# Optimization experiments

Hardware: AMD Instinct MI355X
Metric: run time of the kernel (lower is better)

Reference implementation:

```python
import jax, jax.numpy as jnp
import numpy as np

B, L, D = 2, 256, 256  # batch, length, raw feature dim (W dims are D+1)

def setup_inputs() -> dict:
    key = jax.random.key(0)
    k1, k2, k3, kw = jax.random.split(key, 4)
    layer1 = jax.random.normal(k1, (B, L, D), dtype=jnp.float32)
    layer2 = jax.random.normal(k2, (B, L, D), dtype=jnp.float32)
    layer3 = jax.random.normal(k3, (B, L, D), dtype=jnp.float32)
    # xavier_normal_ for a 3D tensor: fan_in = D+1 * (D+1) receptive? torch treats
    # dim0 as fan_out-ish; we just use a matched-scale gaussian (correctness of the
    # contraction math is what matters for the kernel baseline).
    std = float(np.sqrt(2.0 / ((D + 1) + (D + 1) * (D + 1))))
    W = jax.random.normal(kw, (D + 1, D + 1, D + 1), dtype=jnp.float32) * std
    return {"layer1": layer1, "layer2": layer2, "layer3": layer3, "W": W}

def _append_ones(x):
    ones = jnp.ones(x.shape[:2] + (1,), dtype=x.dtype)
    return jnp.concatenate([x, ones], axis=-1)

def reference(layer1, layer2, layer3, W):
    l1 = _append_ones(layer1)  # [n, L, a]
    l2 = _append_ones(layer2)  # [n, L, b]
    l3 = _append_ones(layer3)  # [n, L, c]
    # Chained contraction: nia,abc -> nibc ; nibc,njb -> nijc ; nijc,nkc -> nijk
    t = jnp.einsum('nia,abc->nibc', l1, W)
    t = jnp.einsum('nibc,njb->nijc', t, l2)
    out = jnp.einsum('nijc,nkc->nijk', t, l3)
    return out
```

## Files before the change

kernel.cpp:

```cpp
#include <hip/hip_runtime.h>

typedef unsigned short u16;
typedef __attribute__((ext_vector_type(8))) short bf16x8;
typedef __attribute__((ext_vector_type(4))) float f32x4;

#define GLOAD_LDS16(gsrc, ldst)                                               \
  __builtin_amdgcn_global_load_lds(                                           \
      (const __attribute__((address_space(1))) void*)(gsrc),                  \
      (__attribute__((address_space(3))) void*)(ldst), 16, 0, 0)

#define LDSOFF(p) \
  ((unsigned)(uintptr_t)(__attribute__((address_space(3))) const void*)(p))

#define SB0 __builtin_amdgcn_sched_barrier(0)

__device__ __forceinline__ u16 f2bf(float x) {
  unsigned u = __float_as_uint(x);
  u = (u + 0x7FFFu + ((u >> 16) & 1u)) >> 16;
  return (u16)u;
}

__global__ void prep_l_kernel(const float* __restrict__ l1,
                              const float* __restrict__ l2,
                              const float* __restrict__ l3,
                              u16* __restrict__ o1, u16* __restrict__ o2,
                              u16* __restrict__ o3) {
  int idx = blockIdx.x * 256 + threadIdx.x;
  const int NR = 512 * 288;
  if (idx >= 3 * NR) return;
  int which = idx / NR, rem = idx - which * NR;
  int r = rem / 288, p = rem - r * 288;
  const float* s = which == 0 ? l1 : which == 1 ? l2 : l3;
  u16* d = which == 0 ? o1 : which == 1 ? o2 : o3;
  float v = (p < 256) ? s[r * 256 + p] : (p == 256 ? 1.0f : 0.0f);
  d[rem] = f2bf(v);
}

__global__ void prep_w_kernel(const float* __restrict__ W, u16* __restrict__ W2) {
  __shared__ float tile[32][33];
  const int a0 = blockIdx.x * 32, c0 = blockIdx.y * 32, b = blockIdx.z;
  const int t = threadIdx.x;
#pragma unroll
  for (int p = 0; p < 4; ++p) {
    int idx = t + p * 256;
    int cl = idx & 31, r = idx >> 5;
    int a = a0 + r, c = c0 + cl;
    float v = 0.0f;
    if (a < 257 && b < 257 && c < 257) v = W[((long)a * 257 + b) * 257 + c];
    tile[r][cl] = v;
  }
  __syncthreads();
#pragma unroll
  for (int p = 0; p < 4; ++p) {
    int idx = t + p * 256;
    int al = idx & 31, ccl = idx >> 5;
    W2[((long)(c0 + ccl) * 288 + b) * 288 + (a0 + al)] = f2bf(tile[al][ccl]);
  }
}

__global__ __launch_bounds__(256, 4) void gemm_nt(
    const u16* __restrict__ A, const u16* __restrict__ B, u16* __restrict__ C,
    int K, int lda, int ldb, int ldc) {
  __shared__ u16 As[2][4096];
  __shared__ u16 Bs[2][4096];
  const int t = threadIdx.x;
  const int bid = blockIdx.x;
  const int xcd = bid & 7, sq = bid >> 3;
  const int nt = xcd * 81 + (sq >> 2);
  const int mt = sq & 3;
  const int m0 = mt * 128, n0 = nt * 128;
  const int lane = t & 63;
  const int w = t >> 6;
  const int wr = (w >> 1) * 64, wc = (w & 1) * 64;
  const int r16 = lane & 15;
  const int cgrp = lane >> 4;
  const int rr = cgrp * 4;
  const unsigned ABase = LDSOFF(&As[0][0]);
  const unsigned BBase = LDSOFF(&Bs[0][0]);
  (void)K;

  const u16* PA = A + (long)m0 * lda;
  const u16* PB = B + (long)n0 * ldb;

#define STG(buf, k0)                                                          \
  {                                                                           \
    _Pragma("unroll") for (int _p = 0; _p < 2; ++_p) {                        \
      int _q = t + _p * 256;                                                  \
      int _r = _q >> 2, _g = (_q & 3) ^ ((_r >> 1) & 3);                      \
      GLOAD_LDS16(PA + (long)_r * lda + (k0) + _g * 8, &As[buf][_q * 8]);     \
      GLOAD_LDS16(PB + (long)_r * ldb + (k0) + _g * 8, &Bs[buf][_q * 8]);     \
    }                                                                         \
  }

  f32x4 acc[4][4];
  const f32x4 zero = {0.f, 0.f, 0.f, 0.f};
#pragma unroll
  for (int i = 0; i < 4; ++i)
#pragma unroll
    for (int j = 0; j < 4; ++j) acc[i][j] = zero;

  STG(0, 0);

#define GCOL(NI)                                                              \
  __builtin_amdgcn_s_setprio(1);                                              \
  acc[0][NI] = __builtin_amdgcn_mfma_f32_16x16x32_bf16(af[0], bf[NI], acc[0][NI], 0, 0, 0); \
  acc[1][NI] = __builtin_amdgcn_mfma_f32_16x16x32_bf16(af[1], bf[NI], acc[1][NI], 0, 0, 0); \
  acc[2][NI] = __builtin_amdgcn_mfma_f32_16x16x32_bf16(af[2], bf[NI], acc[2][NI], 0, 0, 0); \
  acc[3][NI] = __builtin_amdgcn_mfma_f32_16x16x32_bf16(af[3], bf[NI], acc[3][NI], 0, 0, 0); \
  __builtin_amdgcn_s_setprio(0);                                              \
  SB0;

#define GSTEP(KS, NW)                                                         \
  {                                                                           \
    if ((KS) < 8) STG(((KS) + 1) & 1, ((KS) + 1) * 32);                       \
    asm volatile("s_waitcnt vmcnt(" #NW ")" ::: "memory");                    \
    SB0;                                                                      \
    __builtin_amdgcn_s_barrier();                                             \
    SB0;                                                                      \
    bf16x8 af[4], bf[4];                                                      \
    _Pragma("unroll") for (int mi = 0; mi < 4; ++mi) {                        \
      int R = wr + mi * 16 + r16;                                             \
      unsigned ao = ABase + (unsigned)(((((KS) & 1) * 4096) + R * 32 +        \
                                       ((cgrp ^ ((R >> 1) & 3)) * 8)) * 2);   \
      asm volatile("ds_read_b128 %0, %1" : "=v"(af[mi]) : "v"(ao));           \
    }                                                                         \
    _Pragma("unroll") for (int ni = 0; ni < 4; ++ni) {                        \
      int R = wc + ni * 16 + r16;                                             \
      unsigned ao = BBase + (unsigned)(((((KS) & 1) * 4096) + R * 32 +        \
                                       ((cgrp ^ ((R >> 1) & 3)) * 8)) * 2);   \
      asm volatile("ds_read_b128 %0, %1" : "=v"(bf[ni]) : "v"(ao));           \
    }                                                                         \
    SB0;                                                                      \
    asm volatile("s_waitcnt lgkmcnt(3)" ::: "memory"); SB0;                   \
    GCOL(0)                                                                   \
    asm volatile("s_waitcnt lgkmcnt(2)" ::: "memory"); SB0;                   \
    GCOL(1)                                                                   \
    asm volatile("s_waitcnt lgkmcnt(1)" ::: "memory"); SB0;                   \
    GCOL(2)                                                                   \
    asm volatile("s_waitcnt lgkmcnt(0)" ::: "memory"); SB0;                   \
    GCOL(3)                                                                   \
  }

  GSTEP(0, 4) GSTEP(1, 4) GSTEP(2, 4) GSTEP(3, 4) GSTEP(4, 4)
  GSTEP(5, 4) GSTEP(6, 4) GSTEP(7, 4) GSTEP(8, 0)
#undef GSTEP
#undef GCOL
#undef STG

#pragma unroll
  for (int mi = 0; mi < 4; ++mi) {
    int gm = m0 + wr + mi * 16 + rr;
#pragma unroll
    for (int ni = 0; ni < 4; ++ni) {
      int gc = n0 + wc + ni * 16 + r16;
#pragma unroll
      for (int r = 0; r < 4; ++r)
        C[(long)(gm + r) * ldc + gc] = f2bf(acc[mi][ni][r]);
    }
  }
}

__global__ __launch_bounds__(512, 2) void fused23(
    const u16* __restrict__ l2b, const u16* __restrict__ l3b,
    const u16* __restrict__ T1, float* __restrict__ out) {
  __shared__ u16 S[128 * 296];
  __shared__ u16 Bst[4][288 * 32];
  const int t = threadIdx.x;
  const int lane = t & 63;
  const int w = t >> 6;

  const int bid = blockIdx.x;
  const int xcd = bid & 7;
  const int seq = bid >> 3;
  const int ni = xcd * 64 + (seq >> 1);
  const int half = seq & 1;
  const int n = ni >> 8;

  const int r16 = lane & 15;
  const int cgrp = lane >> 4;
  const int kb = cgrp * 8;
  const int rr = cgrp * 4;
  const f32x4 zero = {0.f, 0.f, 0.f, 0.f};

  const u16* A2 = l2b + (long)n * 73728 + (long)(half * 128) * 288;
  const u16* BT = T1 + (long)ni * 82944;
  const u16* B3 = l3b + (long)n * 73728;
  const unsigned BOF = LDSOFF(&Bst[0][0]);
  const unsigned SOF = LDSOFF(&S[0]);

#define ISSUE_A(buf, kk)                                                      \
  {                                                                           \
    int q1 = w * 144 + lane;                                                  \
    int r1 = q1 >> 2, g1 = (q1 & 3) ^ ((r1 >> 1) & 3);                        \
    GLOAD_LDS16(BT + (long)r1 * 288 + (kk) * 32 + g1 * 8, &Bst[(buf)][q1 * 8]); \
    int q2 = q1 + 64;                                                         \
    int r2 = q2 >> 2, g2 = (q2 & 3) ^ ((r2 >> 1) & 3);                        \
    GLOAD_LDS16(BT + (long)r2 * 288 + (kk) * 32 + g2 * 8, &Bst[(buf)][q2 * 8]); \
    if (lane < 16) {                                                          \
      int q3 = w * 144 + 128 + lane;                                          \
      int r3 = q3 >> 2, g3 = (q3 & 3) ^ ((r3 >> 1) & 3);                      \
      GLOAD_LDS16(BT + (long)r3 * 288 + (kk) * 32 + g3 * 8, &Bst[(buf)][q3 * 8]); \
    }                                                                         \
  }
#define ISSUE_B(buf, kk)                                                      \
  {                                                                           \
    int q1 = w * 128 + lane;                                                  \
    int r1 = q1 >> 2, g1 = (q1 & 3) ^ ((r1 >> 1) & 3);                        \
    GLOAD_LDS16(B3 + (long)r1 * 288 + (kk) * 32 + g1 * 8, &Bst[(buf)][q1 * 8]); \
    int q2 = q1 + 64;                                                         \
    int r2 = q2 >> 2, g2 = (q2 & 3) ^ ((r2 >> 1) & 3);                        \
    GLOAD_LDS16(B3 + (long)r2 * 288 + (kk) * 32 + g2 * 8, &Bst[(buf)][q2 * 8]); \
  }

  {
    const int wm = w & 3, wn = w >> 2;
    f32x4 acc[2][9];
#pragma unroll
    for (int i = 0; i < 2; ++i)
#pragma unroll
      for (int j = 0; j < 9; ++j) acc[i][j] = zero;

    bf16x8 afr[18];
#pragma unroll
    for (int k = 0; k < 9; ++k)
#pragma unroll
      for (int mi = 0; mi < 2; ++mi)
        afr[k * 2 + mi] = *(const bf16x8*)(A2 +
            (long)(wm * 32 + mi * 16 + r16) * 288 + k * 32 + kb);
    SB0;

    ISSUE_A(0, 0);
    ISSUE_A(1, 1);

#define FA_MM(NJ)                                                             \
  __builtin_amdgcn_s_setprio(1);                                              \
  acc[0][NJ] = __builtin_amdgcn_mfma_f32_16x16x32_bf16(afc0, bf[NJ], acc[0][NJ], 0, 0, 0); \
  acc[1][NJ] = __builtin_amdgcn_mfma_f32_16x16x32_bf16(afc1, bf[NJ], acc[1][NJ], 0, 0, 0); \
  __builtin_amdgcn_s_setprio(0);

#define FA_STEP(K, NW)                                                        \
  {                                                                           \
    if ((K) + 2 <= 8) ISSUE_A(((K) + 2) & 3, (K) + 2);                        \
    asm volatile("s_waitcnt vmcnt(" #NW ")" ::: "memory");                    \
    SB0;                                                                      \
    __builtin_amdgcn_s_barrier();                                             \
    SB0;                                                                      \
    bf16x8 bf[9];                                                             \
    _Pragma("unroll") for (int nj = 0; nj < 9; ++nj) {                        \
      const int R = wn * 144 + nj * 16 + r16;                                 \
      unsigned ao = BOF + (unsigned)((((K) & 3) * 9216 + R * 32 +             \
                                      ((cgrp ^ ((R >> 1) & 3)) * 8)) * 2);    \
      asm volatile("ds_read_b128 %0, %1" : "=v"(bf[nj]) : "v"(ao));           \
    }                                                                         \
    SB0;                                                                      \
    const bf16x8 afc0 = afr[(K) * 2 + 0], afc1 = afr[(K) * 2 + 1];            \
    asm volatile("s_waitcnt lgkmcnt(6)" ::: "memory"); SB0;                   \
    FA_MM(0) FA_MM(1) FA_MM(2) SB0;                                           \
    asm volatile("s_waitcnt lgkmcnt(3)" ::: "memory"); SB0;                   \
    FA_MM(3) FA_MM(4) FA_MM(5) SB0;                                           \
    asm volatile("s_waitcnt lgkmcnt(0)" ::: "memory"); SB0;                   \
    FA_MM(6) FA_MM(7) FA_MM(8) SB0;                                           \
  }
    FA_STEP(0, 6) FA_STEP(1, 6) FA_STEP(2, 6) FA_STEP(3, 6) FA_STEP(4, 6)
    FA_STEP(5, 6) FA_STEP(6, 6) FA_STEP(7, 3) FA_STEP(8, 0)
#undef FA_STEP
#undef FA_MM

    __syncthreads();
    ISSUE_B(0, 0);
    ISSUE_B(1, 1);
#pragma unroll
    for (int mi = 0; mi < 2; ++mi)
#pragma unroll
      for (int nj = 0; nj < 9; ++nj)
#pragma unroll
        for (int q = 0; q < 4; ++q)
          S[(wm * 32 + mi * 16 + rr + q) * 296 + wn * 144 + nj * 16 + r16] =
              f2bf(acc[mi][nj][q]);
  }
  __syncthreads();

  {
    const int wm = w & 1, wn = w >> 1;
    f32x4 acc[4][4];
#pragma unroll
    for (int i = 0; i < 4; ++i)
#pragma unroll
      for (int j = 0; j < 4; ++j) acc[i][j] = zero;

#define FB_MM(NI)                                                             \
  __builtin_amdgcn_s_setprio(1);                                              \
  acc[0][NI] = __builtin_amdgcn_mfma_f32_16x16x32_bf16(af[0], bf[NI], acc[0][NI], 0, 0, 0); \
  acc[1][NI] = __builtin_amdgcn_mfma_f32_16x16x32_bf16(af[1], bf[NI], acc[1][NI], 0, 0, 0); \
  acc[2][NI] = __builtin_amdgcn_mfma_f32_16x16x32_bf16(af[2], bf[NI], acc[2][NI], 0, 0, 0); \
  acc[3][NI] = __builtin_amdgcn_mfma_f32_16x16x32_bf16(af[3], bf[NI], acc[3][NI], 0, 0, 0); \
  __builtin_amdgcn_s_setprio(0);                                              \
  SB0;

#define FB_STEP(K, NW)                                                        \
  {                                                                           \
    if ((K) + 2 <= 8) ISSUE_B(((K) + 2) & 3, (K) + 2);                        \
    asm volatile("s_waitcnt vmcnt(" #NW ")" ::: "memory");                    \
    SB0;                                                                      \
    __builtin_amdgcn_s_barrier();                                             \
    SB0;                                                                      \
    bf16x8 af[4], bf[4];                                                      \
    _Pragma("unroll") for (int mi = 0; mi < 4; ++mi) {                        \
      unsigned ao = SOF + (unsigned)(((wm * 64 + mi * 16 + r16) * 296 +       \
                                      (K) * 32 + kb) * 2);                    \
      asm volatile("ds_read_b128 %0, %1" : "=v"(af[mi]) : "v"(ao));           \
    }                                                                         \
    _Pragma("unroll") for (int nj = 0; nj < 4; ++nj) {                        \
      const int R = wn * 64 + nj * 16 + r16;                                  \
      unsigned ao = BOF + (unsigned)((((K) & 3) * 9216 + R * 32 +             \
                                      ((cgrp ^ ((R >> 1) & 3)) * 8)) * 2);    \
      asm volatile("ds_read_b128 %0, %1" : "=v"(bf[nj]) : "v"(ao));           \
    }                                                                         \
    SB0;                                                                      \
    asm volatile("s_waitcnt lgkmcnt(3)" ::: "memory"); SB0;                   \
    FB_MM(0)                                                                  \
    asm volatile("s_waitcnt lgkmcnt(2)" ::: "memory"); SB0;                   \
    FB_MM(1)                                                                  \
    asm volatile("s_waitcnt lgkmcnt(1)" ::: "memory"); SB0;                   \
    FB_MM(2)                                                                  \
    asm volatile("s_waitcnt lgkmcnt(0)" ::: "memory"); SB0;                   \
    FB_MM(3)                                                                  \
  }
    FB_STEP(0, 4) FB_STEP(1, 4) FB_STEP(2, 4) FB_STEP(3, 4) FB_STEP(4, 4)
    FB_STEP(5, 4) FB_STEP(6, 4) FB_STEP(7, 2) FB_STEP(8, 0)
#undef FB_STEP
#undef FB_MM

    float* O = out + (long)ni * 65536 + (long)(half * 128 + wm * 64) * 256 + wn * 64;
#pragma unroll
    for (int mi = 0; mi < 4; ++mi)
#pragma unroll
      for (int nj = 0; nj < 4; ++nj)
#pragma unroll
        for (int q = 0; q < 4; ++q)
          O[(long)(mi * 16 + rr + q) * 256 + nj * 16 + r16] = acc[mi][nj][q];
  }
#undef ISSUE_A
#undef ISSUE_B
}

extern "C" void kernel_launch(void* const* d_in, const int* in_sizes, int n_in,
                              void* d_out, int out_size, void* d_ws, size_t ws_size,
                              hipStream_t stream) {
  const float* l1 = (const float*)d_in[0];
  const float* l2 = (const float*)d_in[1];
  const float* l3 = (const float*)d_in[2];
  const float* W = (const float*)d_in[3];
  float* out = (float*)d_out;
  char* ws = (char*)d_ws;

  const long LB = 512L * 288 * 2;
  u16* l1b = (u16*)ws;
  u16* l2b = (u16*)(ws + LB);
  u16* l3b = (u16*)(ws + 2 * LB);
  u16* T1 = (u16*)(ws + 3 * LB);
  u16* W2 = (u16*)d_out;

  prep_l_kernel<<<1728, 256, 0, stream>>>(l1, l2, l3, l1b, l2b, l3b);

  dim3 gw(9, 9, 288);
  prep_w_kernel<<<gw, 256, 0, stream>>>(W, W2);

  gemm_nt<<<2592, 256, 0, stream>>>(l1b, W2, T1, 288, 288, 288, 82944);

  fused23<<<1024, 512, 0, stream>>>(l2b, l3b, T1, out);
}
```

Before: 159.1 us.

## Retile W transpose, resplit fused kernel, and simplify prefetch pipelines

The W transpose kernel moves to 96x96 tiles with packed 32-bit bf16 stores. The GEMM and fused kernels switch from deep prefetch (vmcnt-tracked, 2-ahead with 4 buffers) to a double buffer with a full vmcnt(0) wait. The next-stage load is now issued after the LDS reads. The fused kernel is split into 2048 blocks of 256 threads, each covering 64 rows instead of 128, and gemm launch bounds drop to 3 waves per EU. Together these trade prefetch depth for lower LDS use and higher occupancy, at the cost of exposed load latency and re-reading T1 four times instead of twice.

```diff
diff --git a/kernel.cpp b/kernel.cpp
--- a/kernel.cpp
+++ b/kernel.cpp
@@ -36,38 +36,42 @@
   d[rem] = f2bf(v);
 }
 
-__global__ void prep_w_kernel(const float* __restrict__ W, u16* __restrict__ W2) {
-  __shared__ float tile[32][33];
-  const int a0 = blockIdx.x * 32, c0 = blockIdx.y * 32, b = blockIdx.z;
+__global__ __launch_bounds__(256, 2) void prep_w_kernel(
+    const float* __restrict__ W, u16* __restrict__ W2) {
+  __shared__ float tile[96][97];
+  const int a0 = blockIdx.x * 96, c0 = blockIdx.y * 96, b = blockIdx.z;
   const int t = threadIdx.x;
-#pragma unroll
-  for (int p = 0; p < 4; ++p) {
-    int idx = t + p * 256;
-    int cl = idx & 31, r = idx >> 5;
-    int a = a0 + r, c = c0 + cl;
+  const bool bok = (b < 257);
+#pragma unroll
+  for (int i = 0; i < 36; ++i) {
+    int idx = t + i * 256;
+    int ar = idx / 96, cc = idx - ar * 96;
+    int a = a0 + ar, c = c0 + cc;
     float v = 0.0f;
-    if (a < 257 && b < 257 && c < 257) v = W[((long)a * 257 + b) * 257 + c];
-    tile[r][cl] = v;
+    if (bok && a < 257 && c < 257) v = W[((long)a * 257 + b) * 257 + c];
+    tile[ar][cc] = v;
   }
   __syncthreads();
 #pragma unroll
-  for (int p = 0; p < 4; ++p) {
-    int idx = t + p * 256;
-    int al = idx & 31, ccl = idx >> 5;
-    W2[((long)(c0 + ccl) * 288 + b) * 288 + (a0 + al)] = f2bf(tile[al][ccl]);
-  }
-}
-
-__global__ __launch_bounds__(256, 4) void gemm_nt(
+  for (int i = 0; i < 18; ++i) {
+    int idx = t + i * 256;
+    int cr = idx / 48, ap = (idx - cr * 48) * 2;
+    unsigned pk = (unsigned)f2bf(tile[ap][cr]) |
+                  ((unsigned)f2bf(tile[ap + 1][cr]) << 16);
+    *(unsigned*)(&W2[((long)(c0 + cr) * 288 + b) * 288 + a0 + ap]) = pk;
+  }
+}
+
+__global__ __launch_bounds__(256, 3) void gemm_nt(
     const u16* __restrict__ A, const u16* __restrict__ B, u16* __restrict__ C,
     int K, int lda, int ldb, int ldc) {
   __shared__ u16 As[2][4096];
   __shared__ u16 Bs[2][4096];
   const int t = threadIdx.x;
   const int bid = blockIdx.x;
-  const int xcd = bid & 7, sq = bid >> 3;
-  const int nt = xcd * 81 + (sq >> 2);
-  const int mt = sq & 3;
+  const int xcd = bid & 7, s = bid >> 3;
+  const int nt = xcd * 81 + (s >> 2);
+  const int mt = s & 3;
   const int m0 = mt * 128, n0 = nt * 128;
   const int lane = t & 63;
   const int w = t >> 6;
@@ -103,17 +107,15 @@
 
 #define GCOL(NI)                                                              \
   __builtin_amdgcn_s_setprio(1);                                              \
-  acc[0][NI] = __builtin_amdgcn_mfma_f32_16x16x32_bf16(af[0], bf[NI], acc[0][NI], 0, 0, 0); \
-  acc[1][NI] = __builtin_amdgcn_mfma_f32_16x16x32_bf16(af[1], bf[NI], acc[1][NI], 0, 0, 0); \
-  acc[2][NI] = __builtin_amdgcn_mfma_f32_16x16x32_bf16(af[2], bf[NI], acc[2][NI], 0, 0, 0); \
-  acc[3][NI] = __builtin_amdgcn_mfma_f32_16x16x32_bf16(af[3], bf[NI], acc[3][NI], 0, 0, 0); \
+  _Pragma("unroll") for (int _mi = 0; _mi < 4; ++_mi)                         \
+    acc[_mi][NI] = __builtin_amdgcn_mfma_f32_16x16x32_bf16(                   \
+        af[_mi], bf[NI], acc[_mi][NI], 0, 0, 0);                              \
   __builtin_amdgcn_s_setprio(0);                                              \
   SB0;
 
-#define GSTEP(KS, NW)                                                         \
-  {                                                                           \
-    if ((KS) < 8) STG(((KS) + 1) & 1, ((KS) + 1) * 32);                       \
-    asm volatile("s_waitcnt vmcnt(" #NW ")" ::: "memory");                    \
+#define GSTEP(KS)                                                             \
+  {                                                                           \
+    asm volatile("s_waitcnt vmcnt(0)" ::: "memory");                          \
     SB0;                                                                      \
     __builtin_amdgcn_s_barrier();                                             \
     SB0;                                                                      \
@@ -130,6 +132,8 @@
                                        ((cgrp ^ ((R >> 1) & 3)) * 8)) * 2);   \
       asm volatile("ds_read_b128 %0, %1" : "=v"(bf[ni]) : "v"(ao));           \
     }                                                                         \
+    SB0;                                                                      \
+    if ((KS) < 8) STG(((KS) + 1) & 1, ((KS) + 1) * 32);                       \
     SB0;                                                                      \
     asm volatile("s_waitcnt lgkmcnt(3)" ::: "memory"); SB0;                   \
     GCOL(0)                                                                   \
@@ -141,8 +145,8 @@
     GCOL(3)                                                                   \
   }
 
-  GSTEP(0, 4) GSTEP(1, 4) GSTEP(2, 4) GSTEP(3, 4) GSTEP(4, 4)
-  GSTEP(5, 4) GSTEP(6, 4) GSTEP(7, 4) GSTEP(8, 0)
+  GSTEP(0) GSTEP(1) GSTEP(2) GSTEP(3) GSTEP(4)
+  GSTEP(5) GSTEP(6) GSTEP(7) GSTEP(8)
 #undef GSTEP
 #undef GCOL
 #undef STG
@@ -160,11 +164,11 @@
   }
 }
 
-__global__ __launch_bounds__(512, 2) void fused23(
+__global__ __launch_bounds__(256, 2) void fused23(
     const u16* __restrict__ l2b, const u16* __restrict__ l3b,
     const u16* __restrict__ T1, float* __restrict__ out) {
-  __shared__ u16 S[128 * 296];
-  __shared__ u16 Bst[4][288 * 32];
+  __shared__ u16 S[64 * 296];
+  __shared__ u16 Bst[2][288 * 32];
   const int t = threadIdx.x;
   const int lane = t & 63;
   const int w = t >> 6;
@@ -172,8 +176,8 @@
   const int bid = blockIdx.x;
   const int xcd = bid & 7;
   const int seq = bid >> 3;
-  const int ni = xcd * 64 + (seq >> 1);
-  const int half = seq & 1;
+  const int ni = xcd * 64 + (seq >> 2);
+  const int q = seq & 3;
   const int n = ni >> 8;
 
   const int r16 = lane & 15;
@@ -182,7 +186,7 @@
   const int rr = cgrp * 4;
   const f32x4 zero = {0.f, 0.f, 0.f, 0.f};
 
-  const u16* A2 = l2b + (long)n * 73728 + (long)(half * 128) * 288;
+  const u16* A2 = l2b + (long)n * 73728 + (long)(q * 64) * 288;
   const u16* BT = T1 + (long)ni * 82944;
   const u16* B3 = l3b + (long)n * 73728;
   const unsigned BOF = LDSOFF(&Bst[0][0]);
@@ -190,35 +194,34 @@
 
 #define ISSUE_A(buf, kk)                                                      \
   {                                                                           \
-    int q1 = w * 144 + lane;                                                  \
-    int r1 = q1 >> 2, g1 = (q1 & 3) ^ ((r1 >> 1) & 3);                        \
-    GLOAD_LDS16(BT + (long)r1 * 288 + (kk) * 32 + g1 * 8, &Bst[(buf)][q1 * 8]); \
-    int q2 = q1 + 64;                                                         \
-    int r2 = q2 >> 2, g2 = (q2 & 3) ^ ((r2 >> 1) & 3);                        \
-    GLOAD_LDS16(BT + (long)r2 * 288 + (kk) * 32 + g2 * 8, &Bst[(buf)][q2 * 8]); \
-    if (lane < 16) {                                                          \
-      int q3 = w * 144 + 128 + lane;                                          \
-      int r3 = q3 >> 2, g3 = (q3 & 3) ^ ((r3 >> 1) & 3);                      \
-      GLOAD_LDS16(BT + (long)r3 * 288 + (kk) * 32 + g3 * 8, &Bst[(buf)][q3 * 8]); \
+    _Pragma("unroll") for (int _p = 0; _p < 5; ++_p) {                        \
+      int _q = t + _p * 256;                                                  \
+      if (_q < 1152) {                                                        \
+        int _r = _q >> 2, _g = (_q & 3) ^ ((_r >> 1) & 3);                    \
+        GLOAD_LDS16(BT + (long)_r * 288 + (kk) * 32 + _g * 8,                 \
+                    &Bst[(buf)][_q * 8]);                                     \
+      }                                                                       \
     }                                                                         \
   }
 #define ISSUE_B(buf, kk)                                                      \
   {                                                                           \
-    int q1 = w * 128 + lane;                                                  \
-    int r1 = q1 >> 2, g1 = (q1 & 3) ^ ((r1 >> 1) & 3);                        \
-    GLOAD_LDS16(B3 + (long)r1 * 288 + (kk) * 32 + g1 * 8, &Bst[(buf)][q1 * 8]); \
-    int q2 = q1 + 64;                                                         \
-    int r2 = q2 >> 2, g2 = (q2 & 3) ^ ((r2 >> 1) & 3);                        \
-    GLOAD_LDS16(B3 + (long)r2 * 288 + (kk) * 32 + g2 * 8, &Bst[(buf)][q2 * 8]); \
+    _Pragma("unroll") for (int _p = 0; _p < 4; ++_p) {                        \
+      int _q = t + _p * 256;                                                  \
+      int _r = _q >> 2, _g = (_q & 3) ^ ((_r >> 1) & 3);                      \
+      GLOAD_LDS16(B3 + (long)_r * 288 + (kk) * 32 + _g * 8,                   \
+                  &Bst[(buf)][_q * 8]);                                       \
+    }                                                                         \
   }
 
   {
-    const int wm = w & 3, wn = w >> 2;
+    const int wm = w & 1, wn = w >> 1;
     f32x4 acc[2][9];
 #pragma unroll
     for (int i = 0; i < 2; ++i)
 #pragma unroll
       for (int j = 0; j < 9; ++j) acc[i][j] = zero;
+
+    ISSUE_A(0, 0);
 
     bf16x8 afr[18];
 #pragma unroll
@@ -228,9 +231,6 @@
         afr[k * 2 + mi] = *(const bf16x8*)(A2 +
             (long)(wm * 32 + mi * 16 + r16) * 288 + k * 32 + kb);
     SB0;
-
-    ISSUE_A(0, 0);
-    ISSUE_A(1, 1);
 
 #define FA_MM(NJ)                                                             \
   __builtin_amdgcn_s_setprio(1);                                              \
@@ -238,20 +238,21 @@
   acc[1][NJ] = __builtin_amdgcn_mfma_f32_16x16x32_bf16(afc1, bf[NJ], acc[1][NJ], 0, 0, 0); \
   __builtin_amdgcn_s_setprio(0);
 
-#define FA_STEP(K, NW)                                                        \
-  {                                                                           \
-    if ((K) + 2 <= 8) ISSUE_A(((K) + 2) & 3, (K) + 2);                        \
-    asm volatile("s_waitcnt vmcnt(" #NW ")" ::: "memory");                    \
+#define FA_STEP(K)                                                            \
+  {                                                                           \
+    asm volatile("s_waitcnt vmcnt(0)" ::: "memory");                          \
     SB0;                                                                      \
     __builtin_amdgcn_s_barrier();                                             \
     SB0;                                                                      \
     bf16x8 bf[9];                                                             \
     _Pragma("unroll") for (int nj = 0; nj < 9; ++nj) {                        \
       const int R = wn * 144 + nj * 16 + r16;                                 \
-      unsigned ao = BOF + (unsigned)((((K) & 3) * 9216 + R * 32 +             \
+      unsigned ao = BOF + (unsigned)((((K) & 1) * 9216 + R * 32 +             \
                                       ((cgrp ^ ((R >> 1) & 3)) * 8)) * 2);    \
       asm volatile("ds_read_b128 %0, %1" : "=v"(bf[nj]) : "v"(ao));           \
     }                                                                         \
+    SB0;                                                                      \
+    if ((K) < 8) ISSUE_A(((K) + 1) & 1, (K) + 1);                             \
     SB0;                                                                      \
     const bf16x8 afc0 = afr[(K) * 2 + 0], afc1 = afr[(K) * 2 + 1];            \
     asm volatile("s_waitcnt lgkmcnt(6)" ::: "memory"); SB0;                   \
@@ -261,27 +262,25 @@
     asm volatile("s_waitcnt lgkmcnt(0)" ::: "memory"); SB0;                   \
     FA_MM(6) FA_MM(7) FA_MM(8) SB0;                                           \
   }
-    FA_STEP(0, 6) FA_STEP(1, 6) FA_STEP(2, 6) FA_STEP(3, 6) FA_STEP(4, 6)
-    FA_STEP(5, 6) FA_STEP(6, 6) FA_STEP(7, 3) FA_STEP(8, 0)
+    FA_STEP(0) FA_STEP(1) FA_STEP(2) FA_STEP(3) FA_STEP(4)
+    FA_STEP(5) FA_STEP(6) FA_STEP(7) FA_STEP(8)
 #undef FA_STEP
 #undef FA_MM
 
     __syncthreads();
     ISSUE_B(0, 0);
-    ISSUE_B(1, 1);
 #pragma unroll
     for (int mi = 0; mi < 2; ++mi)
 #pragma unroll
       for (int nj = 0; nj < 9; ++nj)
 #pragma unroll
-        for (int q = 0; q < 4; ++q)
-          S[(wm * 32 + mi * 16 + rr + q) * 296 + wn * 144 + nj * 16 + r16] =
-              f2bf(acc[mi][nj][q]);
+        for (int qq = 0; qq < 4; ++qq)
+          S[(wm * 32 + mi * 16 + rr + qq) * 296 + wn * 144 + nj * 16 + r16] =
+              f2bf(acc[mi][nj][qq]);
   }
   __syncthreads();
 
   {
-    const int wm = w & 1, wn = w >> 1;
     f32x4 acc[4][4];
 #pragma unroll
     for (int i = 0; i < 4; ++i)
@@ -290,32 +289,32 @@
 
 #define FB_MM(NI)                                                             \
   __builtin_amdgcn_s_setprio(1);                                              \
-  acc[0][NI] = __builtin_amdgcn_mfma_f32_16x16x32_bf16(af[0], bf[NI], acc[0][NI], 0, 0, 0); \
-  acc[1][NI] = __builtin_amdgcn_mfma_f32_16x16x32_bf16(af[1], bf[NI], acc[1][NI], 0, 0, 0); \
-  acc[2][NI] = __builtin_amdgcn_mfma_f32_16x16x32_bf16(af[2], bf[NI], acc[2][NI], 0, 0, 0); \
-  acc[3][NI] = __builtin_amdgcn_mfma_f32_16x16x32_bf16(af[3], bf[NI], acc[3][NI], 0, 0, 0); \
+  _Pragma("unroll") for (int _mi = 0; _mi < 4; ++_mi)                         \
+    acc[_mi][NI] = __builtin_amdgcn_mfma_f32_16x16x32_bf16(                   \
+        af[_mi], bf[NI], acc[_mi][NI], 0, 0, 0);                              \
   __builtin_amdgcn_s_setprio(0);                                              \
   SB0;
 
-#define FB_STEP(K, NW)                                                        \
-  {                                                                           \
-    if ((K) + 2 <= 8) ISSUE_B(((K) + 2) & 3, (K) + 2);                        \
-    asm volatile("s_waitcnt vmcnt(" #NW ")" ::: "memory");                    \
+#define FB_STEP(K)                                                            \
+  {                                                                           \
+    asm volatile("s_waitcnt vmcnt(0)" ::: "memory");                          \
     SB0;                                                                      \
     __builtin_amdgcn_s_barrier();                                             \
     SB0;                                                                      \
     bf16x8 af[4], bf[4];                                                      \
     _Pragma("unroll") for (int mi = 0; mi < 4; ++mi) {                        \
-      unsigned ao = SOF + (unsigned)(((wm * 64 + mi * 16 + r16) * 296 +       \
+      unsigned ao = SOF + (unsigned)(((mi * 16 + r16) * 296 +                 \
                                       (K) * 32 + kb) * 2);                    \
       asm volatile("ds_read_b128 %0, %1" : "=v"(af[mi]) : "v"(ao));           \
     }                                                                         \
     _Pragma("unroll") for (int nj = 0; nj < 4; ++nj) {                        \
-      const int R = wn * 64 + nj * 16 + r16;                                  \
-      unsigned ao = BOF + (unsigned)((((K) & 3) * 9216 + R * 32 +             \
+      const int R = w * 64 + nj * 16 + r16;                                   \
+      unsigned ao = BOF + (unsigned)((((K) & 1) * 9216 + R * 32 +             \
                                       ((cgrp ^ ((R >> 1) & 3)) * 8)) * 2);    \
       asm volatile("ds_read_b128 %0, %1" : "=v"(bf[nj]) : "v"(ao));           \
     }                                                                         \
+    SB0;                                                                      \
+    if ((K) < 8) ISSUE_B(((K) + 1) & 1, (K) + 1);                             \
     SB0;                                                                      \
     asm volatile("s_waitcnt lgkmcnt(3)" ::: "memory"); SB0;                   \
     FB_MM(0)                                                                  \
@@ -326,19 +325,19 @@
     asm volatile("s_waitcnt lgkmcnt(0)" ::: "memory"); SB0;                   \
     FB_MM(3)                                                                  \
   }
-    FB_STEP(0, 4) FB_STEP(1, 4) FB_STEP(2, 4) FB_STEP(3, 4) FB_STEP(4, 4)
-    FB_STEP(5, 4) FB_STEP(6, 4) FB_STEP(7, 2) FB_STEP(8, 0)
+    FB_STEP(0) FB_STEP(1) FB_STEP(2) FB_STEP(3) FB_STEP(4)
+    FB_STEP(5) FB_STEP(6) FB_STEP(7) FB_STEP(8)
 #undef FB_STEP
 #undef FB_MM
 
-    float* O = out + (long)ni * 65536 + (long)(half * 128 + wm * 64) * 256 + wn * 64;
+    float* O = out + (long)ni * 65536 + (long)(q * 64) * 256 + w * 64;
 #pragma unroll
     for (int mi = 0; mi < 4; ++mi)
 #pragma unroll
       for (int nj = 0; nj < 4; ++nj)
 #pragma unroll
-        for (int q = 0; q < 4; ++q)
-          O[(long)(mi * 16 + rr + q) * 256 + nj * 16 + r16] = acc[mi][nj][q];
+        for (int qq = 0; qq < 4; ++qq)
+          O[(long)(mi * 16 + rr + qq) * 256 + nj * 16 + r16] = acc[mi][nj][qq];
   }
 #undef ISSUE_A
 #undef ISSUE_B
@@ -363,10 +362,10 @@
 
   prep_l_kernel<<<1728, 256, 0, stream>>>(l1, l2, l3, l1b, l2b, l3b);
 
-  dim3 gw(9, 9, 288);
+  dim3 gw(3, 3, 288);
   prep_w_kernel<<<gw, 256, 0, stream>>>(W, W2);
 
   gemm_nt<<<2592, 256, 0, stream>>>(l1b, W2, T1, 288, 288, 288, 82944);
 
-  fused23<<<1024, 512, 0, stream>>>(l2b, l3b, T1, out);
-}
+  fused23<<<2048, 256, 0, stream>>>(l2b, l3b, T1, out);
+}
```

Result: slower. 183.5 us (+15.3%).
